# Kernel tuning notes

Measured on AMD Instinct MI355X. Metric: run time of the kernel, lower is better.

Reference implementation:

```python
import jax, jax.numpy as jnp
import numpy as np

HIDDEN = 1024
FFN = 4096
NUM_EXPERTS = 8
TOKENS = 4096


def setup_inputs() -> dict:
    key = jax.random.key(0)
    k1, k2, k3, k4 = jax.random.split(key, 4)
    x = jax.random.normal(k1, (TOKENS, HIDDEN), dtype=jnp.float32)
    router_weight = jax.random.normal(k2, (HIDDEN, NUM_EXPERTS), dtype=jnp.float32) * 0.02
    w1 = jax.random.normal(k3, (HIDDEN, FFN * NUM_EXPERTS), dtype=jnp.float32) * 0.02
    w2 = jax.random.normal(k4, (FFN * NUM_EXPERTS, HIDDEN), dtype=jnp.float32) * 0.02
    return {"x": x, "router_weight": router_weight, "w1": w1, "w2": w2, "top_k": 2}


def reference(x, router_weight, w1, w2, top_k):
    T, H = x.shape
    E = router_weight.shape[1]
    F = w1.shape[1] // E

    # Router: fp32 logits -> softmax -> top-k gating (sparse gates in dense [T, E] form)
    logits = x.astype(jnp.float32) @ router_weight  # [T, E]
    probs = jax.nn.softmax(logits, axis=-1)
    top_vals, top_idx = jax.lax.top_k(probs, top_k)  # [T, k]
    gates = jnp.zeros((T, E), dtype=probs.dtype).at[
        jnp.arange(T)[:, None], top_idx
    ].set(top_vals)  # [T, E], zero for non-selected experts

    # Per-expert FFN (expert-blocked weight layout: columns [e*F:(e+1)*F])
    w1e = w1.reshape(H, E, F)          # [H, E, F]
    w2e = w2.reshape(E, F, H)          # [E, F, H]
    h = jax.nn.gelu(jnp.einsum('th,hef->etf', x, w1e), approximate=False)  # [E, T, F]
    y = jnp.einsum('etf,efh->eth', h, w2e)  # [E, T, H]

    # Combine: gate-weighted sum over experts
    out = jnp.einsum('te,eth->th', gates.astype(y.dtype), y)  # [T, H]
    return out
```

## Files before the change

kernel.cpp:

```cpp
#include <hip/hip_runtime.h>
#include <hip/hip_bf16.h>

#define T_TOKENS 4096
#define HID 1024
#define FFN_ 4096
#define NE 8
#define MAXROWS 10240
#define MAXTILES 40

typedef unsigned short u16;
typedef __bf16 bf16x8 __attribute__((ext_vector_type(8)));
typedef float f32x4 __attribute__((ext_vector_type(4)));
typedef u16 u16x8 __attribute__((ext_vector_type(8)));

__device__ __forceinline__ u16 f2bf(float f) {
  __hip_bfloat16 h = __float2bfloat16(f);
  return *reinterpret_cast<u16*>(&h);
}

__device__ __forceinline__ void gload16(const void* g, void* l) {
  __builtin_amdgcn_global_load_lds(
      (const __attribute__((address_space(1))) void*)g,
      (__attribute__((address_space(3))) void*)l, 16, 0, 0);
}

#define WAIT_VM6() asm volatile("s_waitcnt vmcnt(6)" ::: "memory")
#define WAIT_VM0() asm volatile("s_waitcnt vmcnt(0)" ::: "memory")
#define BARRIER()  asm volatile("s_barrier" ::: "memory")

__global__ __launch_bounds__(256) void router_kernel(
    const float* __restrict__ x, const float* __restrict__ rw,
    int* __restrict__ sel, float* __restrict__ gsel, u16* __restrict__ xb) {
  int token = blockIdx.x * 4 + (threadIdx.x >> 6);
  int lane = threadIdx.x & 63;
  const float* xr = x + (size_t)token * HID;
  u16* xbr = xb + (size_t)token * HID;
  float acc[8];
#pragma unroll
  for (int e = 0; e < 8; e++) acc[e] = 0.f;
  for (int h = lane; h < HID; h += 64) {
    float xv = xr[h];
    xbr[h] = f2bf(xv);
    float4 r0 = *(const float4*)(rw + h * 8);
    float4 r1 = *(const float4*)(rw + h * 8 + 4);
    acc[0] += xv * r0.x; acc[1] += xv * r0.y; acc[2] += xv * r0.z; acc[3] += xv * r0.w;
    acc[4] += xv * r1.x; acc[5] += xv * r1.y; acc[6] += xv * r1.z; acc[7] += xv * r1.w;
  }
#pragma unroll
  for (int e = 0; e < 8; e++) {
#pragma unroll
    for (int o = 32; o > 0; o >>= 1) acc[e] += __shfl_down(acc[e], o);
  }
  if (lane == 0) {
    float mx = acc[0];
#pragma unroll
    for (int e = 1; e < 8; e++) mx = fmaxf(mx, acc[e]);
    float p[8], s = 0.f;
#pragma unroll
    for (int e = 0; e < 8; e++) { p[e] = expf(acc[e] - mx); s += p[e]; }
    float v0 = -1.f; int i0 = 0;
#pragma unroll
    for (int e = 0; e < 8; e++) if (p[e] > v0) { v0 = p[e]; i0 = e; }
    float v1 = -1.f; int i1 = 0;
#pragma unroll
    for (int e = 0; e < 8; e++) if (e != i0 && p[e] > v1) { v1 = p[e]; i1 = e; }
    float inv = 1.f / s;
    sel[token * 2] = i0;     gsel[token * 2] = v0 * inv;
    sel[token * 2 + 1] = i1; gsel[token * 2 + 1] = v1 * inv;
  }
}

__global__ __launch_bounds__(256) void hist_fill_kernel(
    const int* __restrict__ sel, int* __restrict__ counts,
    int* __restrict__ perm, float* __restrict__ grow) {
  __shared__ int lc[NE];
  if (threadIdx.x < NE) lc[threadIdx.x] = 0;
  __syncthreads();
  int gid = blockIdx.x * 256 + threadIdx.x;
  if (gid < T_TOKENS * 2) atomicAdd(&lc[sel[gid]], 1);
  if (gid < MAXROWS) { perm[gid] = -1; grow[gid] = 0.f; }
  __syncthreads();
  if (threadIdx.x < NE && lc[threadIdx.x] > 0)
    atomicAdd(&counts[threadIdx.x], lc[threadIdx.x]);
}

__global__ void base_kernel(const int* __restrict__ counts, int* __restrict__ cursor,
                            int* __restrict__ tilemap) {
  if (threadIdx.x == 0) {
    int base = 0;
    for (int e = 0; e < NE; e++) {
      cursor[e] = base;
      int padded = (base + counts[e] + 255) & ~255;
      for (int t = base >> 8; t < (padded >> 8); t++) tilemap[t] = e;
      base = padded;
    }
    for (int t = base >> 8; t < MAXTILES; t++) tilemap[t] = 0;
  }
}

__global__ __launch_bounds__(256) void scatter_kernel(
    const int* __restrict__ sel, const float* __restrict__ gsel,
    int* __restrict__ cursor, int* __restrict__ perm, float* __restrict__ grow) {
  int p = blockIdx.x * 256 + threadIdx.x;
  int e = sel[p];
  int pos = atomicAdd(&cursor[e], 1);
  perm[pos] = p >> 1;
  grow[pos] = gsel[p];
}

__global__ __launch_bounds__(256) void transpose_w1(const float* __restrict__ w1, u16* __restrict__ w1t) {
  __shared__ float tile[64][65];
  int c0 = blockIdx.x * 64;
  int r0 = blockIdx.y * 64;
  int t = threadIdx.x;
  int ci = (t & 15) * 4;
  int ri = t >> 4;
#pragma unroll
  for (int rr = 0; rr < 64; rr += 16) {
    float4 v = *(const float4*)(w1 + (size_t)(r0 + ri + rr) * 32768 + c0 + ci);
    tile[ri + rr][ci] = v.x; tile[ri + rr][ci + 1] = v.y;
    tile[ri + rr][ci + 2] = v.z; tile[ri + rr][ci + 3] = v.w;
  }
  __syncthreads();
  int j = t >> 2;
  int q = t & 3;
  u16x8 o0, o1;
#pragma unroll
  for (int k = 0; k < 8; k++) o0[k] = f2bf(tile[q * 16 + k][j]);
#pragma unroll
  for (int k = 0; k < 8; k++) o1[k] = f2bf(tile[q * 16 + 8 + k][j]);
  u16* dst = w1t + (size_t)(c0 + j) * 1024 + r0 + q * 16;
  *(u16x8*)dst = o0;
  *(u16x8*)(dst + 8) = o1;
}

__global__ __launch_bounds__(256) void transpose_w2(const float* __restrict__ w2, u16* __restrict__ w2t) {
  __shared__ float tile[64][65];
  int fb = blockIdx.x;
  int h0 = blockIdx.y * 64;
  int e = fb >> 6;
  int f0 = (fb & 63) * 64;
  int t = threadIdx.x;
  int ci = (t & 15) * 4;
  int ri = t >> 4;
#pragma unroll
  for (int rr = 0; rr < 64; rr += 16) {
    float4 v = *(const float4*)(w2 + (size_t)(fb * 64 + ri + rr) * 1024 + h0 + ci);
    tile[ri + rr][ci] = v.x; tile[ri + rr][ci + 1] = v.y;
    tile[ri + rr][ci + 2] = v.z; tile[ri + rr][ci + 3] = v.w;
  }
  __syncthreads();
  int j = t >> 2;
  int q = t & 3;
  u16x8 o0, o1;
#pragma unroll
  for (int k = 0; k < 8; k++) o0[k] = f2bf(tile[q * 16 + k][j]);
#pragma unroll
  for (int k = 0; k < 8; k++) o1[k] = f2bf(tile[q * 16 + 8 + k][j]);
  u16* dst = w2t + (size_t)e * 4194304 + (size_t)(h0 + j) * 4096 + f0 + q * 16;
  *(u16x8*)dst = o0;
  *(u16x8*)(dst + 8) = o1;
}

__global__ __launch_bounds__(512, 1) void gemm1_kernel(
    const u16* __restrict__ xb, const u16* __restrict__ w1t,
    const int* __restrict__ perm, const float* __restrict__ grow,
    const int* __restrict__ tilemap, u16* __restrict__ hbuf,
    const u16* __restrict__ zp) {
  int bid = blockIdx.x;
  int xcd = bid & 7, pos = bid >> 3;
  int nt = pos / 5;
  int mt = xcd * 5 + (pos - nt * 5);
  int e = tilemap[mt];
  int row0 = mt * 256;
  int t = threadIdx.x, lane = t & 63, wave = t >> 6;
  __shared__ u16 As[3][256 * 64], Bs[3][128 * 64];

  const u16* asrc[4]; int astep[4];
  const u16* bsrc[2];
#pragma unroll
  for (int i = 0; i < 4; i++) {
    int chunk = i * 512 + t, row = chunk >> 3, c = chunk & 7;
    int cs = c ^ (row & 7);
    int tok = perm[row0 + row];
    if (tok >= 0) { asrc[i] = xb + (size_t)tok * 1024 + cs * 8; astep[i] = 64; }
    else { asrc[i] = zp + cs * 8; astep[i] = 0; }
  }
#pragma unroll
  for (int i = 0; i < 2; i++) {
    int chunk = i * 512 + t, row = chunk >> 3, c = chunk & 7;
    int cs = c ^ (row & 7);
    bsrc[i] = w1t + (size_t)e * 4194304 + (size_t)(nt * 128 + row) * 1024 + cs * 8;
  }

  f32x4 acc[4][4] = {};
  int wm = wave >> 1, wn = wave & 1;
  int r = lane & 15, kg = lane >> 4;

  auto stage = [&](int s) {
#pragma unroll
    for (int i = 0; i < 4; i++)
      gload16(asrc[i], (char*)&As[s][0] + i * 8192 + wave * 1024);
#pragma unroll
    for (int i = 0; i < 2; i++)
      gload16(bsrc[i], (char*)&Bs[s][0] + i * 8192 + wave * 1024);
#pragma unroll
    for (int i = 0; i < 4; i++) asrc[i] += astep[i];
#pragma unroll
    for (int i = 0; i < 2; i++) bsrc[i] += 64;
  };
  auto compute = [&](int s) {
    const char* Ab = (const char*)&As[s][0];
    const char* Bb = (const char*)&Bs[s][0];
#pragma unroll
    for (int kk = 0; kk < 2; kk++) {
      int kb = kk * 64 + kg * 16;
      bf16x8 af[4], bfr[4];
#pragma unroll
      for (int mi = 0; mi < 4; mi++) {
        int rr = wm * 64 + mi * 16 + r;
        af[mi] = *(const bf16x8*)(Ab + rr * 128 + (kb ^ ((rr & 7) << 4)));
      }
#pragma unroll
      for (int ni = 0; ni < 4; ni++) {
        int rr = wn * 64 + ni * 16 + r;
        bfr[ni] = *(const bf16x8*)(Bb + rr * 128 + (kb ^ ((rr & 7) << 4)));
      }
      __builtin_amdgcn_s_setprio(1);
#pragma unroll
      for (int mi = 0; mi < 4; mi++)
#pragma unroll
        for (int ni = 0; ni < 4; ni++)
          acc[mi][ni] = __builtin_amdgcn_mfma_f32_16x16x32_bf16(af[mi], bfr[ni], acc[mi][ni], 0, 0, 0);
      __builtin_amdgcn_s_setprio(0);
    }
  };

  stage(0);
  stage(1);
  for (int kt = 0; kt < 16; kt++) {
    if (kt == 15) { WAIT_VM0(); } else { WAIT_VM6(); }
    BARRIER();
    compute(kt % 3);
    if (kt < 14) stage((kt + 2) % 3);
  }

  float g[4][4];
#pragma unroll
  for (int mi = 0; mi < 4; mi++)
#pragma unroll
    for (int j = 0; j < 4; j++)
      g[mi][j] = grow[row0 + wm * 64 + mi * 16 + kg * 4 + j];
#pragma unroll
  for (int mi = 0; mi < 4; mi++)
#pragma unroll
    for (int ni = 0; ni < 4; ni++)
#pragma unroll
      for (int j = 0; j < 4; j++) {
        int rl = wm * 64 + mi * 16 + kg * 4 + j;
        int col = nt * 128 + wn * 64 + ni * 16 + r;
        float v = acc[mi][ni][j];
        float ge = 0.5f * v * (1.0f + erff(v * 0.7071067811865475f)) * g[mi][j];
        hbuf[(size_t)(row0 + rl) * 4096 + col] = f2bf(ge);
      }
}

__global__ __launch_bounds__(512, 1) void gemm2_kernel(
    const u16* __restrict__ hbuf, const u16* __restrict__ w2t,
    const int* __restrict__ perm, const int* __restrict__ tilemap,
    float* __restrict__ out) {
  int bid = blockIdx.x;
  int xcd = bid & 7, pos = bid >> 3;
  int c32 = pos / 5;
  int mt = xcd * 5 + (pos - c32 * 5);
  int ksp = c32 >> 3;
  int nt = c32 & 7;
  int e = tilemap[mt];
  int row0 = mt * 256;
  int t = threadIdx.x, lane = t & 63, wave = t >> 6;
  __shared__ u16 As[3][256 * 64], Bs[3][128 * 64];

  const u16* asrc[4];
  const u16* bsrc[2];
#pragma unroll
  for (int i = 0; i < 4; i++) {
    int chunk = i * 512 + t, row = chunk >> 3, c = chunk & 7;
    int cs = c ^ (row & 7);
    asrc[i] = hbuf + (size_t)(row0 + row) * 4096 + (size_t)ksp * 1024 + cs * 8;
  }
#pragma unroll
  for (int i = 0; i < 2; i++) {
    int chunk = i * 512 + t, row = chunk >> 3, c = chunk & 7;
    int cs = c ^ (row & 7);
    bsrc[i] = w2t + (size_t)e * 4194304 + (size_t)(nt * 128 + row) * 4096 + (size_t)ksp * 1024 + cs * 8;
  }

  f32x4 acc[4][4] = {};
  int wm = wave >> 1, wn = wave & 1;
  int r = lane & 15, kg = lane >> 4;

  auto stage = [&](int s) {
#pragma unroll
    for (int i = 0; i < 4; i++)
      gload16(asrc[i], (char*)&As[s][0] + i * 8192 + wave * 1024);
#pragma unroll
    for (int i = 0; i < 2; i++)
      gload16(bsrc[i], (char*)&Bs[s][0] + i * 8192 + wave * 1024);
#pragma unroll
    for (int i = 0; i < 4; i++) asrc[i] += 64;
#pragma unroll
    for (int i = 0; i < 2; i++) bsrc[i] += 64;
  };
  auto compute = [&](int s) {
    const char* Ab = (const char*)&As[s][0];
    const char* Bb = (const char*)&Bs[s][0];
#pragma unroll
    for (int kk = 0; kk < 2; kk++) {
      int kb = kk * 64 + kg * 16;
      bf16x8 af[4], bfr[4];
#pragma unroll
      for (int mi = 0; mi < 4; mi++) {
        int rr = wm * 64 + mi * 16 + r;
        af[mi] = *(const bf16x8*)(Ab + rr * 128 + (kb ^ ((rr & 7) << 4)));
      }
#pragma unroll
      for (int ni = 0; ni < 4; ni++) {
        int rr = wn * 64 + ni * 16 + r;
        bfr[ni] = *(const bf16x8*)(Bb + rr * 128 + (kb ^ ((rr & 7) << 4)));
      }
      __builtin_amdgcn_s_setprio(1);
#pragma unroll
      for (int mi = 0; mi < 4; mi++)
#pragma unroll
        for (int ni = 0; ni < 4; ni++)
          acc[mi][ni] = __builtin_amdgcn_mfma_f32_16x16x32_bf16(af[mi], bfr[ni], acc[mi][ni], 0, 0, 0);
      __builtin_amdgcn_s_setprio(0);
    }
  };

  stage(0);
  stage(1);
  for (int kt = 0; kt < 16; kt++) {
    if (kt == 15) { WAIT_VM0(); } else { WAIT_VM6(); }
    BARRIER();
    compute(kt % 3);
    if (kt < 14) stage((kt + 2) % 3);
  }

  int tok[4][4];
#pragma unroll
  for (int mi = 0; mi < 4; mi++)
#pragma unroll
    for (int j = 0; j < 4; j++)
      tok[mi][j] = perm[row0 + wm * 64 + mi * 16 + kg * 4 + j];
#pragma unroll
  for (int mi = 0; mi < 4; mi++)
#pragma unroll
    for (int ni = 0; ni < 4; ni++)
#pragma unroll
      for (int j = 0; j < 4; j++) {
        if (tok[mi][j] >= 0) {
          int col = nt * 128 + wn * 64 + ni * 16 + r;
          atomicAdd(out + (size_t)tok[mi][j] * 1024 + col, acc[mi][ni][j]);
        }
      }
}

extern "C" void kernel_launch(void* const* d_in, const int* in_sizes, int n_in,
                              void* d_out, int out_size, void* d_ws, size_t ws_size,
                              hipStream_t stream) {
  const float* x  = (const float*)d_in[0];
  const float* rw = (const float*)d_in[1];
  const float* w1 = (const float*)d_in[2];
  const float* w2 = (const float*)d_in[3];
  float* out = (float*)d_out;
  char* ws = (char*)d_ws;

  size_t off = 0;
  auto take = [&](size_t n) { char* p = ws + off; off += (n + 255) & ~255ull; return p; };
  u16* w1t   = (u16*)take(8ull * 4096 * 1024 * 2);
  u16* w2t   = (u16*)take(8ull * 4096 * 1024 * 2);
  u16* xb    = (u16*)take((size_t)T_TOKENS * HID * 2);
  u16* hbuf  = (u16*)take((size_t)MAXROWS * FFN_ * 2);
  int* sel   = (int*)take(T_TOKENS * 2 * 4);
  float* gsel = (float*)take(T_TOKENS * 2 * 4);
  int* perm  = (int*)take(MAXROWS * 4);
  float* grow = (float*)take(MAXROWS * 4);
  int* tmap  = (int*)take(MAXTILES * 4);
  int* counts = (int*)take(NE * 4);
  int* cursor = (int*)take(NE * 4);
  u16* zp    = (u16*)take(4096);

  hipMemsetAsync(zp, 0, 4096, stream);
  hipMemsetAsync(counts, 0, NE * 4, stream);
  hipMemsetAsync(out, 0, (size_t)T_TOKENS * HID * 4, stream);

  transpose_w1<<<dim3(512, 16), 256, 0, stream>>>(w1, w1t);
  transpose_w2<<<dim3(512, 16), 256, 0, stream>>>(w2, w2t);
  router_kernel<<<dim3(T_TOKENS / 4), 256, 0, stream>>>(x, rw, sel, gsel, xb);
  hist_fill_kernel<<<dim3(MAXROWS / 256), 256, 0, stream>>>(sel, counts, perm, grow);
  base_kernel<<<dim3(1), 64, 0, stream>>>(counts, cursor, tmap);
  scatter_kernel<<<dim3(T_TOKENS * 2 / 256), 256, 0, stream>>>(sel, gsel, cursor, perm, grow);
  gemm1_kernel<<<dim3(1280), 512, 0, stream>>>(xb, w1t, perm, grow, tmap, hbuf, zp);
  gemm2_kernel<<<dim3(1280), 512, 0, stream>>>(hbuf, w2t, perm, tmap, out);
}
```

Before: 440.4 us.

## Enlarge GEMM tiles to 256x256 with double-buffered phased load/compute interleave

Both expert GEMM kernels move from 256x128 output tiles with a 3-stage buffer to 256x256 tiles with 2-stage double buffering. Each K-step is split into four compute phases, and half-tile global-to-LDS loads are issued between them. B fragments are held in registers across the phases. The aim is to raise arithmetic intensity per tile, halve the grid, and overlap loads with MFMA at a finer grain. In exchange it uses more accumulator registers, adds more barriers per K-step, and leaves fewer blocks (640) on the 256 CUs.

```diff
diff --git a/kernel.cpp b/kernel.cpp
--- a/kernel.cpp
+++ b/kernel.cpp
@@ -24,7 +24,8 @@
       (__attribute__((address_space(3))) void*)l, 16, 0, 0);
 }
 
-#define WAIT_VM6() asm volatile("s_waitcnt vmcnt(6)" ::: "memory")
+#define WAIT_VM2() asm volatile("s_waitcnt vmcnt(2)" ::: "memory")
+#define WAIT_VM4() asm volatile("s_waitcnt vmcnt(4)" ::: "memory")
 #define WAIT_VM0() asm volatile("s_waitcnt vmcnt(0)" ::: "memory")
 #define BARRIER()  asm volatile("s_barrier" ::: "memory")
 
@@ -174,95 +175,115 @@
   int e = tilemap[mt];
   int row0 = mt * 256;
   int t = threadIdx.x, lane = t & 63, wave = t >> 6;
-  __shared__ u16 As[3][256 * 64], Bs[3][128 * 64];
-
+  __shared__ u16 As[2][256 * 64], Bs[2][256 * 64];
+
+  int trow = t >> 3;
+  int cs = (t & 7) ^ (trow & 7);
   const u16* asrc[4]; int astep[4];
-  const u16* bsrc[2];
+  const u16* bsrc[4];
 #pragma unroll
   for (int i = 0; i < 4; i++) {
-    int chunk = i * 512 + t, row = chunk >> 3, c = chunk & 7;
-    int cs = c ^ (row & 7);
+    int row = i * 64 + trow;
     int tok = perm[row0 + row];
     if (tok >= 0) { asrc[i] = xb + (size_t)tok * 1024 + cs * 8; astep[i] = 64; }
     else { asrc[i] = zp + cs * 8; astep[i] = 0; }
-  }
-#pragma unroll
-  for (int i = 0; i < 2; i++) {
-    int chunk = i * 512 + t, row = chunk >> 3, c = chunk & 7;
-    int cs = c ^ (row & 7);
-    bsrc[i] = w1t + (size_t)e * 4194304 + (size_t)(nt * 128 + row) * 1024 + cs * 8;
-  }
-
-  f32x4 acc[4][4] = {};
-  int wm = wave >> 1, wn = wave & 1;
+    bsrc[i] = w1t + (size_t)e * 4194304 + (size_t)(nt * 256 + row) * 1024 + cs * 8;
+  }
+
+  f32x4 acc[8][4] = {};
+  bf16x8 bq[4][2];
   int r = lane & 15, kg = lane >> 4;
-
-  auto stage = [&](int s) {
-#pragma unroll
-    for (int i = 0; i < 4; i++)
-      gload16(asrc[i], (char*)&As[s][0] + i * 8192 + wave * 1024);
-#pragma unroll
-    for (int i = 0; i < 2; i++)
-      gload16(bsrc[i], (char*)&Bs[s][0] + i * 8192 + wave * 1024);
-#pragma unroll
-    for (int i = 0; i < 4; i++) asrc[i] += astep[i];
-#pragma unroll
-    for (int i = 0; i < 2; i++) bsrc[i] += 64;
-  };
-  auto compute = [&](int s) {
-    const char* Ab = (const char*)&As[s][0];
-    const char* Bb = (const char*)&Bs[s][0];
-#pragma unroll
-    for (int kk = 0; kk < 2; kk++) {
-      int kb = kk * 64 + kg * 16;
-      bf16x8 af[4], bfr[4];
-#pragma unroll
-      for (int mi = 0; mi < 4; mi++) {
-        int rr = wm * 64 + mi * 16 + r;
-        af[mi] = *(const bf16x8*)(Ab + rr * 128 + (kb ^ ((rr & 7) << 4)));
-      }
+  int wm = wave >> 2, wn = wave & 3;
+
+  auto stageB = [&](int d, int half) {
+    char* base = (char*)&Bs[d][0] + half * 16384;
+    gload16(bsrc[half * 2], base + t * 16);
+    gload16(bsrc[half * 2 + 1], base + 8192 + t * 16);
+  };
+  auto stageA = [&](int d, int pair) {
+    char* base = (char*)&As[d][0];
+    if (pair == 0) {
+      gload16(asrc[0], base + t * 16);
+      gload16(asrc[2], base + 16384 + t * 16);
+    } else {
+      gload16(asrc[1], base + 8192 + t * 16);
+      gload16(asrc[3], base + 24576 + t * 16);
+    }
+  };
+  auto adv = [&]() {
+#pragma unroll
+    for (int i = 0; i < 4; i++) { asrc[i] += astep[i]; bsrc[i] += 64; }
+  };
+  auto readB = [&](int d) {
+    const char* Bb = (const char*)&Bs[d][0];
+#pragma unroll
+    for (int ni = 0; ni < 4; ni++)
+#pragma unroll
+      for (int kk = 0; kk < 2; kk++) {
+        int rr = wn * 64 + ni * 16 + r;
+        bq[ni][kk] = *(const bf16x8*)(Bb + rr * 128 + ((kk * 64 + kg * 16) ^ ((rr & 7) << 4)));
+      }
+  };
+  auto phase = [&](int d, int q) {
+    const char* Ab = (const char*)&As[d][0];
+    bf16x8 af[2][2];
+#pragma unroll
+    for (int m2 = 0; m2 < 2; m2++)
+#pragma unroll
+      for (int kk = 0; kk < 2; kk++) {
+        int rr = wm * 128 + (q * 2 + m2) * 16 + r;
+        af[m2][kk] = *(const bf16x8*)(Ab + rr * 128 + ((kk * 64 + kg * 16) ^ ((rr & 7) << 4)));
+      }
+    __builtin_amdgcn_s_setprio(1);
+#pragma unroll
+    for (int m2 = 0; m2 < 2; m2++)
+#pragma unroll
+      for (int ni = 0; ni < 4; ni++)
+#pragma unroll
+        for (int kk = 0; kk < 2; kk++)
+          acc[q * 2 + m2][ni] = __builtin_amdgcn_mfma_f32_16x16x32_bf16(af[m2][kk], bq[ni][kk], acc[q * 2 + m2][ni], 0, 0, 0);
+    __builtin_amdgcn_s_setprio(0);
+  };
+
+  stageB(0, 0); stageB(0, 1); stageA(0, 0); stageA(0, 1);
+  adv();
+  for (int kt = 0; kt < 16; kt++) {
+    int d = kt & 1;
+    bool st = kt < 15;
+    WAIT_VM2(); BARRIER();
+    readB(d);
+    if (st) stageB(d ^ 1, 0);
+    phase(d, 0);
+    BARRIER();
+    if (st) stageB(d ^ 1, 1);
+    phase(d, 1);
+    BARRIER();
+    if (kt == 15) { WAIT_VM0(); } else { WAIT_VM4(); }
+    BARRIER();
+    if (st) stageA(d ^ 1, 0);
+    phase(d, 2);
+    BARRIER();
+    if (st) stageA(d ^ 1, 1);
+    phase(d, 3);
+    if (st) adv();
+    BARRIER();
+  }
+
+#pragma unroll
+  for (int mi = 0; mi < 8; mi++) {
+    int rl = wm * 128 + mi * 16 + kg * 4;
+#pragma unroll
+    for (int j = 0; j < 4; j++) {
+      float gv = grow[row0 + rl + j];
 #pragma unroll
       for (int ni = 0; ni < 4; ni++) {
-        int rr = wn * 64 + ni * 16 + r;
-        bfr[ni] = *(const bf16x8*)(Bb + rr * 128 + (kb ^ ((rr & 7) << 4)));
-      }
-      __builtin_amdgcn_s_setprio(1);
-#pragma unroll
-      for (int mi = 0; mi < 4; mi++)
-#pragma unroll
-        for (int ni = 0; ni < 4; ni++)
-          acc[mi][ni] = __builtin_amdgcn_mfma_f32_16x16x32_bf16(af[mi], bfr[ni], acc[mi][ni], 0, 0, 0);
-      __builtin_amdgcn_s_setprio(0);
+        int col = nt * 256 + wn * 64 + ni * 16 + r;
+        float v = acc[mi][ni][j];
+        float ge = 0.5f * v * (1.0f + erff(v * 0.7071067811865475f)) * gv;
+        hbuf[(size_t)(row0 + rl + j) * 4096 + col] = f2bf(ge);
+      }
     }
-  };
-
-  stage(0);
-  stage(1);
-  for (int kt = 0; kt < 16; kt++) {
-    if (kt == 15) { WAIT_VM0(); } else { WAIT_VM6(); }
-    BARRIER();
-    compute(kt % 3);
-    if (kt < 14) stage((kt + 2) % 3);
-  }
-
-  float g[4][4];
-#pragma unroll
-  for (int mi = 0; mi < 4; mi++)
-#pragma unroll
-    for (int j = 0; j < 4; j++)
-      g[mi][j] = grow[row0 + wm * 64 + mi * 16 + kg * 4 + j];
-#pragma unroll
-  for (int mi = 0; mi < 4; mi++)
-#pragma unroll
-    for (int ni = 0; ni < 4; ni++)
-#pragma unroll
-      for (int j = 0; j < 4; j++) {
-        int rl = wm * 64 + mi * 16 + kg * 4 + j;
-        int col = nt * 128 + wn * 64 + ni * 16 + r;
-        float v = acc[mi][ni][j];
-        float ge = 0.5f * v * (1.0f + erff(v * 0.7071067811865475f)) * g[mi][j];
-        hbuf[(size_t)(row0 + rl) * 4096 + col] = f2bf(ge);
-      }
+  }
 }
 
 __global__ __launch_bounds__(512, 1) void gemm2_kernel(
@@ -271,99 +292,120 @@
     float* __restrict__ out) {
   int bid = blockIdx.x;
   int xcd = bid & 7, pos = bid >> 3;
-  int c32 = pos / 5;
-  int mt = xcd * 5 + (pos - c32 * 5);
-  int ksp = c32 >> 3;
-  int nt = c32 & 7;
+  int c16 = pos / 5;
+  int mt = xcd * 5 + (pos - c16 * 5);
+  int ksp = c16 >> 2;
+  int nt = c16 & 3;
   int e = tilemap[mt];
   int row0 = mt * 256;
   int t = threadIdx.x, lane = t & 63, wave = t >> 6;
-  __shared__ u16 As[3][256 * 64], Bs[3][128 * 64];
-
+  __shared__ u16 As[2][256 * 64], Bs[2][256 * 64];
+
+  int trow = t >> 3;
+  int cs = (t & 7) ^ (trow & 7);
   const u16* asrc[4];
-  const u16* bsrc[2];
+  const u16* bsrc[4];
 #pragma unroll
   for (int i = 0; i < 4; i++) {
-    int chunk = i * 512 + t, row = chunk >> 3, c = chunk & 7;
-    int cs = c ^ (row & 7);
+    int row = i * 64 + trow;
     asrc[i] = hbuf + (size_t)(row0 + row) * 4096 + (size_t)ksp * 1024 + cs * 8;
-  }
-#pragma unroll
-  for (int i = 0; i < 2; i++) {
-    int chunk = i * 512 + t, row = chunk >> 3, c = chunk & 7;
-    int cs = c ^ (row & 7);
-    bsrc[i] = w2t + (size_t)e * 4194304 + (size_t)(nt * 128 + row) * 4096 + (size_t)ksp * 1024 + cs * 8;
-  }
-
-  f32x4 acc[4][4] = {};
-  int wm = wave >> 1, wn = wave & 1;
+    bsrc[i] = w2t + (size_t)e * 4194304 + (size_t)(nt * 256 + row) * 4096 + (size_t)ksp * 1024 + cs * 8;
+  }
+
+  f32x4 acc[8][4] = {};
+  bf16x8 bq[4][2];
   int r = lane & 15, kg = lane >> 4;
-
-  auto stage = [&](int s) {
-#pragma unroll
-    for (int i = 0; i < 4; i++)
-      gload16(asrc[i], (char*)&As[s][0] + i * 8192 + wave * 1024);
-#pragma unroll
-    for (int i = 0; i < 2; i++)
-      gload16(bsrc[i], (char*)&Bs[s][0] + i * 8192 + wave * 1024);
-#pragma unroll
-    for (int i = 0; i < 4; i++) asrc[i] += 64;
-#pragma unroll
-    for (int i = 0; i < 2; i++) bsrc[i] += 64;
-  };
-  auto compute = [&](int s) {
-    const char* Ab = (const char*)&As[s][0];
-    const char* Bb = (const char*)&Bs[s][0];
-#pragma unroll
-    for (int kk = 0; kk < 2; kk++) {
-      int kb = kk * 64 + kg * 16;
-      bf16x8 af[4], bfr[4];
-#pragma unroll
-      for (int mi = 0; mi < 4; mi++) {
-        int rr = wm * 64 + mi * 16 + r;
-        af[mi] = *(const bf16x8*)(Ab + rr * 128 + (kb ^ ((rr & 7) << 4)));
-      }
-#pragma unroll
-      for (int ni = 0; ni < 4; ni++) {
+  int wm = wave >> 2, wn = wave & 3;
+
+  auto stageB = [&](int d, int half) {
+    char* base = (char*)&Bs[d][0] + half * 16384;
+    gload16(bsrc[half * 2], base + t * 16);
+    gload16(bsrc[half * 2 + 1], base + 8192 + t * 16);
+  };
+  auto stageA = [&](int d, int pair) {
+    char* base = (char*)&As[d][0];
+    if (pair == 0) {
+      gload16(asrc[0], base + t * 16);
+      gload16(asrc[2], base + 16384 + t * 16);
+    } else {
+      gload16(asrc[1], base + 8192 + t * 16);
+      gload16(asrc[3], base + 24576 + t * 16);
+    }
+  };
+  auto adv = [&]() {
+#pragma unroll
+    for (int i = 0; i < 4; i++) { asrc[i] += 64; bsrc[i] += 64; }
+  };
+  auto readB = [&](int d) {
+    const char* Bb = (const char*)&Bs[d][0];
+#pragma unroll
+    for (int ni = 0; ni < 4; ni++)
+#pragma unroll
+      for (int kk = 0; kk < 2; kk++) {
         int rr = wn * 64 + ni * 16 + r;
-        bfr[ni] = *(const bf16x8*)(Bb + rr * 128 + (kb ^ ((rr & 7) << 4)));
-      }
-      __builtin_amdgcn_s_setprio(1);
-#pragma unroll
-      for (int mi = 0; mi < 4; mi++)
-#pragma unroll
-        for (int ni = 0; ni < 4; ni++)
-          acc[mi][ni] = __builtin_amdgcn_mfma_f32_16x16x32_bf16(af[mi], bfr[ni], acc[mi][ni], 0, 0, 0);
-      __builtin_amdgcn_s_setprio(0);
+        bq[ni][kk] = *(const bf16x8*)(Bb + rr * 128 + ((kk * 64 + kg * 16) ^ ((rr & 7) << 4)));
+      }
+  };
+  auto phase = [&](int d, int q) {
+    const char* Ab = (const char*)&As[d][0];
+    bf16x8 af[2][2];
+#pragma unroll
+    for (int m2 = 0; m2 < 2; m2++)
+#pragma unroll
+      for (int kk = 0; kk < 2; kk++) {
+        int rr = wm * 128 + (q * 2 + m2) * 16 + r;
+        af[m2][kk] = *(const bf16x8*)(Ab + rr * 128 + ((kk * 64 + kg * 16) ^ ((rr & 7) << 4)));
+      }
+    __builtin_amdgcn_s_setprio(1);
+#pragma unroll
+    for (int m2 = 0; m2 < 2; m2++)
+#pragma unroll
+      for (int ni = 0; ni < 4; ni++)
+#pragma unroll
+        for (int kk = 0; kk < 2; kk++)
+          acc[q * 2 + m2][ni] = __builtin_amdgcn_mfma_f32_16x16x32_bf16(af[m2][kk], bq[ni][kk], acc[q * 2 + m2][ni], 0, 0, 0);
+    __builtin_amdgcn_s_setprio(0);
+  };
+
+  stageB(0, 0); stageB(0, 1); stageA(0, 0); stageA(0, 1);
+  adv();
+  for (int kt = 0; kt < 16; kt++) {
+    int d = kt & 1;
+    bool st = kt < 15;
+    WAIT_VM2(); BARRIER();
+    readB(d);
+    if (st) stageB(d ^ 1, 0);
+    phase(d, 0);
+    BARRIER();
+    if (st) stageB(d ^ 1, 1);
+    phase(d, 1);
+    BARRIER();
+    if (kt == 15) { WAIT_VM0(); } else { WAIT_VM4(); }
+    BARRIER();
+    if (st) stageA(d ^ 1, 0);
+    phase(d, 2);
+    BARRIER();
+    if (st) stageA(d ^ 1, 1);
+    phase(d, 3);
+    if (st) adv();
+    BARRIER();
+  }
+
+#pragma unroll
+  for (int mi = 0; mi < 8; mi++) {
+    int rl = wm * 128 + mi * 16 + kg * 4;
+#pragma unroll
+    for (int j = 0; j < 4; j++) {
+      int tok = perm[row0 + rl + j];
+      if (tok >= 0) {
+#pragma unroll
+        for (int ni = 0; ni < 4; ni++) {
+          int col = nt * 256 + wn * 64 + ni * 16 + r;
+          atomicAdd(out + (size_t)tok * 1024 + col, acc[mi][ni][j]);
+        }
+      }
     }
-  };
-
-  stage(0);
-  stage(1);
-  for (int kt = 0; kt < 16; kt++) {
-    if (kt == 15) { WAIT_VM0(); } else { WAIT_VM6(); }
-    BARRIER();
-    compute(kt % 3);
-    if (kt < 14) stage((kt + 2) % 3);
-  }
-
-  int tok[4][4];
-#pragma unroll
-  for (int mi = 0; mi < 4; mi++)
-#pragma unroll
-    for (int j = 0; j < 4; j++)
-      tok[mi][j] = perm[row0 + wm * 64 + mi * 16 + kg * 4 + j];
-#pragma unroll
-  for (int mi = 0; mi < 4; mi++)
-#pragma unroll
-    for (int ni = 0; ni < 4; ni++)
-#pragma unroll
-      for (int j = 0; j < 4; j++) {
-        if (tok[mi][j] >= 0) {
-          int col = nt * 128 + wn * 64 + ni * 16 + r;
-          atomicAdd(out + (size_t)tok[mi][j] * 1024 + col, acc[mi][ni][j]);
-        }
-      }
+  }
 }
 
 extern "C" void kernel_launch(void* const* d_in, const int* in_sizes, int n_in,
@@ -401,6 +443,6 @@
   hist_fill_kernel<<<dim3(MAXROWS / 256), 256, 0, stream>>>(sel, counts, perm, grow);
   base_kernel<<<dim3(1), 64, 0, stream>>>(counts, cursor, tmap);
   scatter_kernel<<<dim3(T_TOKENS * 2 / 256), 256, 0, stream>>>(sel, gsel, cursor, perm, grow);
-  gemm1_kernel<<<dim3(1280), 512, 0, stream>>>(xb, w1t, perm, grow, tmap, hbuf, zp);
-  gemm2_kernel<<<dim3(1280), 512, 0, stream>>>(hbuf, w2t, perm, tmap, out);
-}
+  gemm1_kernel<<<dim3(640), 512, 0, stream>>>(xb, w1t, perm, grow, tmap, hbuf, zp);
+  gemm2_kernel<<<dim3(640), 512, 0, stream>>>(hbuf, w2t, perm, tmap, out);
+}
```

After: 496.2 us. 12.7% more time.
